# Kernel tuning notes

Measured on AMD Instinct MI355X. Metric: run time of the kernel, lower is better.

The kernel has to match this reference:

```python
import jax, jax.numpy as jnp
import numpy as np

G = 7          # grid size
OBJ_P = 0.3    # fraction of cells containing an object


def _to_xyxy(x, y, w, h, m, n):
    # x pairs with grid index m (dim 2), y with n (dim 3), per the original loop
    cx = (x + m) / G
    cy = (y + n) / G
    return cx - w / 2, cy - h / 2, cx + w / 2, cy + h / 2


def _iou(b1, b2):
    x1a, y1a, x2a, y2a = b1
    x1b, y1b, x2b, y2b = b2
    iw = jnp.maximum(jnp.minimum(x2a, x2b) - jnp.maximum(x1a, x1b), 0.0)
    ih = jnp.maximum(jnp.minimum(y2a, y2b) - jnp.maximum(y1a, y1b), 0.0)
    inter = iw * ih
    a1 = (x2a - x1a) * (y2a - y1a)
    a2 = (x2b - x1b) * (y2b - y1b)
    union = a1 + a2 - inter
    return jnp.where(inter > 0, inter / union, 0.0)


def setup_inputs() -> dict:
    key = jax.random.key(0)
    k1, k2, k3 = jax.random.split(key, 3)
    B = 32768
    pred = jax.random.uniform(k1, (B, 30, G, G), dtype=jnp.float32)
    labels = jax.random.uniform(k2, (B, 30, G, G), dtype=jnp.float32)
    obj_mask = jax.random.bernoulli(k3, OBJ_P, (B, G, G)).astype(jnp.float32)
    labels = labels.at[:, 4].set(obj_mask)
    return {"pred": pred, "labels": labels}


def reference(pred, labels):
    B = pred.shape[0]
    m = jnp.arange(G, dtype=pred.dtype)[:, None]   # dim 2
    n = jnp.arange(G, dtype=pred.dtype)[None, :]   # dim 3

    obj = labels[:, 4] == 1.0                       # (B,G,G)

    box1 = _to_xyxy(pred[:, 0], pred[:, 1], pred[:, 2], pred[:, 3], m, n)
    box2 = _to_xyxy(pred[:, 5], pred[:, 6], pred[:, 7], pred[:, 8], m, n)
    boxg = _to_xyxy(labels[:, 0], labels[:, 1], labels[:, 2], labels[:, 3], m, n)

    iou1 = _iou(box1, boxg)
    iou2 = _iou(box2, boxg)
    resp1 = iou1 >= iou2

    coor1 = 5.0 * (jnp.sum((pred[:, 0:2] - labels[:, 0:2]) ** 2, axis=1)
                   + jnp.sum((jnp.sqrt(pred[:, 2:4]) - jnp.sqrt(labels[:, 2:4])) ** 2, axis=1))
    coor2 = 5.0 * (jnp.sum((pred[:, 5:7] - labels[:, 5:7]) ** 2, axis=1)
                   + jnp.sum((jnp.sqrt(pred[:, 7:9]) - jnp.sqrt(labels[:, 7:9])) ** 2, axis=1))

    loss_b1 = coor1 + (pred[:, 4] - iou1) ** 2 + 0.5 * (pred[:, 9] - iou2) ** 2
    loss_b2 = coor2 + (pred[:, 9] - iou2) ** 2 + 0.5 * (pred[:, 4] - iou1) ** 2

    cls = jnp.sum((pred[:, 10:] - labels[:, 10:]) ** 2, axis=1)

    obj_loss = jnp.where(resp1, loss_b1, loss_b2) + cls
    noobj_loss = 0.5 * (pred[:, 4] ** 2 + pred[:, 9] ** 2)

    total = jnp.sum(jnp.where(obj, obj_loss, noobj_loss))
    return total / B
```

## Files before the change

kernel.cpp:

```cpp
#include <hip/hip_runtime.h>


#define GRID 7
#define NCH 30
#define CPI (GRID * GRID)

__device__ __forceinline__ float iou_xyxy(float x1a, float y1a, float x2a, float y2a,
                                          float x1b, float y1b, float x2b, float y2b) {
    float iw = fmaxf(fminf(x2a, x2b) - fmaxf(x1a, x1b), 0.0f);
    float ih = fmaxf(fminf(y2a, y2b) - fmaxf(y1a, y1b), 0.0f);
    float inter = iw * ih;
    float a1 = (x2a - x1a) * (y2a - y1a);
    float a2 = (x2b - x1b) * (y2b - y1b);
    float uni = a1 + a2 - inter;
    return inter > 0.0f ? inter / uni : 0.0f;
}

__global__ void __launch_bounds__(256) yolo_loss_kernel(
        const float* __restrict__ pred,
        const float* __restrict__ labels,
        float* __restrict__ out,
        int ncells, float invB) {
    int tid = blockIdx.x * blockDim.x + threadIdx.x;
    float acc = 0.0f;
    if (tid < ncells) {
        int b = tid / CPI;
        int cell = tid - b * CPI;
        int m = cell / GRID;
        int n = cell - m * GRID;

        const float* pb = pred   + (size_t)b * (NCH * CPI) + cell;
        const float* lb = labels + (size_t)b * (NCH * CPI) + cell;

        float p0 = pb[0 * CPI], p1 = pb[1 * CPI], p2 = pb[2 * CPI], p3 = pb[3 * CPI];
        float p4 = pb[4 * CPI], p5 = pb[5 * CPI], p6 = pb[6 * CPI], p7 = pb[7 * CPI];
        float p8 = pb[8 * CPI], p9 = pb[9 * CPI];
        float l0 = lb[0 * CPI], l1 = lb[1 * CPI], l2 = lb[2 * CPI], l3 = lb[3 * CPI];
        float lobj = lb[4 * CPI];
        float l5 = lb[5 * CPI], l6 = lb[6 * CPI], l7 = lb[7 * CPI], l8 = lb[8 * CPI];

        float cls = 0.0f;
        #pragma unroll
        for (int c = 10; c < NCH; ++c) {
            float d = pb[c * CPI] - lb[c * CPI];
            cls += d * d;
        }

        const float inv_g = 1.0f / (float)GRID;
        float fm = (float)m, fn = (float)n;

        float cx = (p0 + fm) * inv_g, cy = (p1 + fn) * inv_g;
        float b1x1 = cx - p2 * 0.5f, b1y1 = cy - p3 * 0.5f;
        float b1x2 = cx + p2 * 0.5f, b1y2 = cy + p3 * 0.5f;
        cx = (p5 + fm) * inv_g; cy = (p6 + fn) * inv_g;
        float b2x1 = cx - p7 * 0.5f, b2y1 = cy - p8 * 0.5f;
        float b2x2 = cx + p7 * 0.5f, b2y2 = cy + p8 * 0.5f;
        cx = (l0 + fm) * inv_g; cy = (l1 + fn) * inv_g;
        float gx1 = cx - l2 * 0.5f, gy1 = cy - l3 * 0.5f;
        float gx2 = cx + l2 * 0.5f, gy2 = cy + l3 * 0.5f;

        float iou1 = iou_xyxy(b1x1, b1y1, b1x2, b1y2, gx1, gy1, gx2, gy2);
        float iou2 = iou_xyxy(b2x1, b2y1, b2x2, b2y2, gx1, gy1, gx2, gy2);
        bool resp1 = iou1 >= iou2;

        float dx = p0 - l0, dy = p1 - l1;
        float dw = sqrtf(p2) - sqrtf(l2), dh = sqrtf(p3) - sqrtf(l3);
        float coor1 = 5.0f * (dx * dx + dy * dy + dw * dw + dh * dh);
        dx = p5 - l5; dy = p6 - l6;
        dw = sqrtf(p7) - sqrtf(l7); dh = sqrtf(p8) - sqrtf(l8);
        float coor2 = 5.0f * (dx * dx + dy * dy + dw * dw + dh * dh);

        float e1 = p4 - iou1, e2 = p9 - iou2;
        float loss_b1 = coor1 + e1 * e1 + 0.5f * e2 * e2;
        float loss_b2 = coor2 + e2 * e2 + 0.5f * e1 * e1;

        float obj_loss = (resp1 ? loss_b1 : loss_b2) + cls;
        float noobj_loss = 0.5f * (p4 * p4 + p9 * p9);

        float contrib = (lobj == 1.0f) ? obj_loss : noobj_loss;
        acc = contrib * invB;
    }

    #pragma unroll
    for (int off = 32; off > 0; off >>= 1)
        acc += __shfl_down(acc, off, 64);

    __shared__ float smem[4];
    int lane = threadIdx.x & 63;
    int wid = threadIdx.x >> 6;
    if (lane == 0) smem[wid] = acc;
    __syncthreads();
    if (threadIdx.x == 0) {
        float v = smem[0] + smem[1] + smem[2] + smem[3];
        atomicAdd(out, v);
    }
}

extern "C" void kernel_launch(void* const* d_in, const int* in_sizes, int n_in,
                              void* d_out, int out_size, void* d_ws, size_t ws_size,
                              hipStream_t stream) {
    const float* pred = (const float*)d_in[0];
    const float* labels = (const float*)d_in[1];
    float* out = (float*)d_out;

    int total = in_sizes[0];
    int B = total / (NCH * CPI);
    int ncells = B * CPI;

    hipMemsetAsync(out, 0, sizeof(float), stream);

    int block = 256;
    int grid = (ncells + block - 1) / block;
    yolo_loss_kernel<<<grid, block, 0, stream>>>(pred, labels, out, ncells, 1.0f / (float)B);
}
```

Baseline: 388.0 us.

## Stage four images per block into LDS with float4 loads

```diff
diff --git a/kernel.cpp b/kernel.cpp
--- a/kernel.cpp
+++ b/kernel.cpp
@@ -4,6 +4,9 @@
 #define GRID 7
 #define NCH 30
 #define CPI (GRID * GRID)
+#define IMG 4
+#define FPI (NCH * CPI)
+#define F4PB (IMG * FPI / 4)
 
 __device__ __forceinline__ float iou_xyxy(float x1a, float y1a, float x2a, float y2a,
                                           float x1b, float y1b, float x2b, float y2b) {
@@ -20,17 +23,27 @@
         const float* __restrict__ pred,
         const float* __restrict__ labels,
         float* __restrict__ out,
-        int ncells, float invB) {
-    int tid = blockIdx.x * blockDim.x + threadIdx.x;
+        float invB) {
+    __shared__ float4 smem[2 * F4PB];
+
+    const float4* pg = (const float4*)pred   + (size_t)blockIdx.x * F4PB;
+    const float4* lg = (const float4*)labels + (size_t)blockIdx.x * F4PB;
+    #pragma unroll
+    for (int i = threadIdx.x; i < 2 * F4PB; i += 256) {
+        smem[i] = (i < F4PB) ? pg[i] : lg[i - F4PB];
+    }
+    __syncthreads();
+
     float acc = 0.0f;
-    if (tid < ncells) {
-        int b = tid / CPI;
-        int cell = tid - b * CPI;
+    int t = threadIdx.x;
+    if (t < IMG * CPI) {
+        int img = t / CPI;
+        int cell = t - img * CPI;
         int m = cell / GRID;
         int n = cell - m * GRID;
 
-        const float* pb = pred   + (size_t)b * (NCH * CPI) + cell;
-        const float* lb = labels + (size_t)b * (NCH * CPI) + cell;
+        const float* pb = (const float*)smem + img * FPI + cell;
+        const float* lb = (const float*)smem + IMG * FPI + img * FPI + cell;
 
         float p0 = pb[0 * CPI], p1 = pb[1 * CPI], p2 = pb[2 * CPI], p3 = pb[3 * CPI];
         float p4 = pb[4 * CPI], p5 = pb[5 * CPI], p6 = pb[6 * CPI], p7 = pb[7 * CPI];
@@ -85,13 +98,13 @@
     for (int off = 32; off > 0; off >>= 1)
         acc += __shfl_down(acc, off, 64);
 
-    __shared__ float smem[4];
+    __shared__ float rsm[4];
     int lane = threadIdx.x & 63;
     int wid = threadIdx.x >> 6;
-    if (lane == 0) smem[wid] = acc;
+    if (lane == 0) rsm[wid] = acc;
     __syncthreads();
     if (threadIdx.x == 0) {
-        float v = smem[0] + smem[1] + smem[2] + smem[3];
+        float v = rsm[0] + rsm[1] + rsm[2] + rsm[3];
         atomicAdd(out, v);
     }
 }
@@ -104,12 +117,9 @@
     float* out = (float*)d_out;
 
     int total = in_sizes[0];
-    int B = total / (NCH * CPI);
-    int ncells = B * CPI;
+    int B = total / FPI;
+    int nblocks = B / IMG;
 
     hipMemsetAsync(out, 0, sizeof(float), stream);
-
-    int block = 256;
-    int grid = (ncells + block - 1) / block;
-    yolo_loss_kernel<<<grid, block, 0, stream>>>(pred, labels, out, ncells, 1.0f / (float)B);
+    yolo_loss_kernel<<<nblocks, 256, 0, stream>>>(pred, labels, out, 1.0f / (float)B);
 }
```

After: 402.7 us. +3.8%, slower.
